# Performance work log

Measured on AMD Instinct MI355X. Metric: run time of the kernel, lower is better.

The kernel has to match this reference:

```python
import jax, jax.numpy as jnp
import numpy as np

EPS = 1e-05
NUM_HEADS = 8
NUM_GROUPS = 32  # min(32, 512 // 4)


def setup_inputs() -> dict:
    key = jax.random.key(0)
    ks = jax.random.split(key, 5)
    B, C, T, X = 4, 512, 16, 2048
    return {
        "x": jax.random.normal(ks[0], (B, C, T, X), dtype=jnp.float32),
        "gn_w": jnp.ones((C,), dtype=jnp.float32),
        "gn_b": jnp.zeros((C,), dtype=jnp.float32),
        "qkv_w": jax.random.normal(ks[1], (3 * C, C), dtype=jnp.float32) * 0.02,
        "qkv_b": jax.random.normal(ks[2], (3 * C,), dtype=jnp.float32) * 0.02,
        "proj_w": jax.random.normal(ks[3], (C, C), dtype=jnp.float32) * 1e-5,
        "proj_b": jnp.zeros((C,), dtype=jnp.float32),
        "pos_emb": jax.random.normal(ks[4], (NUM_HEADS, 2 * T), dtype=jnp.float32) * 1e-5,
    }


def _group_norm(x, w, b):
    B, C, T, X = x.shape
    g = NUM_GROUPS
    xg = x.reshape(B, g, C // g, T, X)
    mu = xg.mean(axis=(2, 3, 4), keepdims=True)
    var = ((xg - mu) ** 2).mean(axis=(2, 3, 4), keepdims=True)
    xn = ((xg - mu) * jax.lax.rsqrt(var + EPS)).reshape(B, C, T, X)
    return xn * w[None, :, None, None] + b[None, :, None, None]


def reference(x, gn_w, gn_b, qkv_w, qkv_b, proj_w, proj_b, pos_emb):
    dtype = x.dtype
    x = x.astype(jnp.float32)
    B, C, T, X = x.shape
    H = NUM_HEADS
    hc = C // H

    xn = _group_norm(x, gn_w, gn_b)
    # 1x1 conv == channel matmul: [B, 3C, T, X]
    qkv = jnp.einsum('oc,bctx->botx', qkv_w, xn) + qkv_b[None, :, None, None]
    # 'b (n heads c) t x -> n (b x) heads t c'
    qkv = qkv.reshape(B, 3, H, hc, T, X)
    qkv = qkv.transpose(1, 0, 5, 2, 4, 3).reshape(3, B * X, H, T, hc)
    q, k, v = qkv[0], qkv[1], qkv[2]

    scale = 1.0 / np.sqrt(hc)
    attn = jnp.einsum('bhqc,bhkc->bhqk', q, k * scale)  # [(B X), H, T, T]

    i = jnp.arange(T)
    pairwise = i[:, None] - i[None, :] + T - 1        # [T, T] in [0, 2T-2]
    rel = pos_emb[:, pairwise]                         # [H, T, T]

    w = jax.nn.softmax(attn + rel[None], axis=-1)
    out = jnp.einsum('bhqk,bhkc->bhcq', w, v)          # [(B X), H, hc, T]
    # '(b x) h c t -> b (h c) t x'
    out = out.reshape(B, X, H, hc, T).transpose(0, 2, 3, 4, 1).reshape(B, C, T, X)

    y = jnp.einsum('oc,bctx->botx', proj_w, out) + proj_b[None, :, None, None]
    return y.astype(dtype)
```

## Files before the change

### kernel.cpp

```cpp
#include <hip/hip_runtime.h>
#include <math.h>

#define EPSV 1e-5f

typedef _Float16 f16;
typedef _Float16 f16x8 __attribute__((ext_vector_type(8)));
typedef _Float16 f16x4 __attribute__((ext_vector_type(4)));
typedef float f32x4 __attribute__((ext_vector_type(4)));

typedef const __attribute__((address_space(1))) void* as1_cvp;
typedef __attribute__((address_space(3))) void* as3_vp;
__device__ __forceinline__ void load_lds16(const void* g, void* l) {
    __builtin_amdgcn_global_load_lds((as1_cvp)g, (as3_vp)l, 16, 0, 0);
}

static constexpr int GROUP_N = 16 * 16 * 2048;

__global__ __launch_bounds__(256) void k_xtstat(const float* __restrict__ x,
                                                f16* __restrict__ xT,
                                                float* __restrict__ psum2,
                                                float* __restrict__ psq2) {
    const int x0 = blockIdx.x * 64;
    const int c0 = blockIdx.y * 64;
    const int b  = blockIdx.z >> 4, t = blockIdx.z & 15;
    const int tid = threadIdx.x;
    __shared__ float tile[64][68];
#pragma unroll
    for (int it = 0; it < 4; ++it) {
        int idx = it * 256 + tid;
        int c = idx >> 4, xq = idx & 15;
        float4 v = *(const float4*)(x + (((size_t)(b * 512 + c0 + c) * 16 + t) * 2048) + x0 + xq * 4);
        tile[c][xq * 4 + 0] = v.x;
        tile[c][xq * 4 + 1] = v.y;
        tile[c][xq * 4 + 2] = v.z;
        tile[c][xq * 4 + 3] = v.w;
    }
    __syncthreads();
#pragma unroll
    for (int it = 0; it < 2; ++it) {
        int idx = it * 256 + tid;
        int xr = idx >> 3, ch = idx & 7;
        f16x8 h;
#pragma unroll
        for (int e = 0; e < 8; ++e) h[e] = (f16)tile[ch * 8 + e][xr];
        *(f16x8*)(xT + (((size_t)(b * 2048 + x0 + xr) * 16 + t) * 512) + c0 + ch * 8) = h;
    }
    {
        const int gg = tid >> 6, lane = tid & 63;
        float s = 0.f, q = 0.f;
#pragma unroll
        for (int i = 0; i < 16; ++i) {
            float v = tile[gg * 16 + i][lane];
            s += v; q += v * v;
        }
#pragma unroll
        for (int off = 32; off > 0; off >>= 1) {
            s += __shfl_down(s, off);
            q += __shfl_down(q, off);
        }
        if (lane == 0) {
            int grp = b * 32 + blockIdx.y * 4 + gg;
            int col = blockIdx.x * 16 + t;
            psum2[grp * 512 + col] = s;
            psq2[grp * 512 + col] = q;
        }
    }
}

__global__ void k_gn_final2(const float* __restrict__ psum2, const float* __restrict__ psq2,
                            float* __restrict__ mu, float* __restrict__ rs) {
    const int t = threadIdx.x;
    float s = 0.f, q = 0.f;
    const float* ps = psum2 + t * 512;
    const float* pq = psq2 + t * 512;
#pragma unroll 4
    for (int i = 0; i < 512; i += 4) {
        float4 a = *(const float4*)(ps + i);
        float4 c = *(const float4*)(pq + i);
        s += a.x + a.y + a.z + a.w;
        q += c.x + c.y + c.z + c.w;
    }
    const float m = s / (float)GROUP_N;
    float v = q / (float)GROUP_N - m * m;
    mu[t] = m;
    rs[t] = 1.0f / sqrtf(v + EPSV);
}

__global__ __launch_bounds__(256) void k_gn_part(const float* __restrict__ x,
                                                 float* __restrict__ psum,
                                                 float* __restrict__ psq) {
    const int blk = blockIdx.x;
    const int tid = threadIdx.x;
    const float* p = x + (size_t)blk * 32768;
    float s = 0.f, q = 0.f;
#pragma unroll
    for (int i = 0; i < 32; ++i) {
        float4 v = *(const float4*)(p + (size_t)(i * 256 + tid) * 4);
        s += v.x + v.y + v.z + v.w;
        q += v.x * v.x + v.y * v.y + v.z * v.z + v.w * v.w;
    }
#pragma unroll
    for (int off = 32; off > 0; off >>= 1) {
        s += __shfl_down(s, off);
        q += __shfl_down(q, off);
    }
    __shared__ float ls[4], lq[4];
    const int wave = tid >> 6, lane = tid & 63;
    if (lane == 0) { ls[wave] = s; lq[wave] = q; }
    __syncthreads();
    if (tid == 0) {
        psum[blk] = ls[0] + ls[1] + ls[2] + ls[3];
        psq[blk]  = lq[0] + lq[1] + lq[2] + lq[3];
    }
}

__global__ void k_gn_final(const float* __restrict__ psum, const float* __restrict__ psq,
                           float* __restrict__ mu, float* __restrict__ rs) {
    const int t = threadIdx.x;
    float s = 0.f, q = 0.f;
#pragma unroll
    for (int i = 0; i < 16; ++i) { s += psum[t * 16 + i]; q += psq[t * 16 + i]; }
    const float m = s / (float)GROUP_N;
    float v = q / (float)GROUP_N - m * m;
    mu[t] = m;
    rs[t] = 1.0f / sqrtf(v + EPSV);
}

__global__ __launch_bounds__(256) void k_fold_sc(const float* __restrict__ gn_w,
                                                 const float* __restrict__ gn_b,
                                                 const float* __restrict__ mu,
                                                 const float* __restrict__ rs,
                                                 float* __restrict__ sc,
                                                 float* __restrict__ beta) {
    const int u = blockIdx.x * 256 + threadIdx.x;
    const int b = u >> 9, c = u & 511;
    const int g = c >> 4;
    const float r = rs[b * 32 + g], m = mu[b * 32 + g];
    const float s = r * gn_w[c];
    sc[u]   = s;
    beta[u] = gn_b[c] - m * s;
}

__global__ __launch_bounds__(256) void k_fold_bias(const float* __restrict__ qkv_w,
                                                   const float* __restrict__ qkv_b,
                                                   const float* __restrict__ beta,
                                                   float* __restrict__ qbias) {
    const int u = blockIdx.x * 256 + threadIdx.x;
    const int b = u / 1536, o = u % 1536;
    float acc = qkv_b[o];
    const float* wr = qkv_w + (size_t)o * 512;
    const float* be = beta + b * 512;
#pragma unroll 4
    for (int c = 0; c < 512; c += 4) {
        float4 w4 = *(const float4*)(wr + c);
        float4 b4 = *(const float4*)(be + c);
        acc += w4.x * b4.x + w4.y * b4.y + w4.z * b4.z + w4.w * b4.w;
    }
    if (o >= 512 && o < 1024) acc *= 0.125f;
    qbias[u] = acc;
}

__global__ __launch_bounds__(256) void k_prep_wb(const float* __restrict__ qkv_w,
                                                 const float* __restrict__ sc,
                                                 f16* __restrict__ w16b) {
    const int id = blockIdx.x * 256 + threadIdx.x;
    const int b  = blockIdx.y;
    const int e0 = id * 4;
    const int o  = e0 >> 9;
    const float ksc = (o >= 512 && o < 1024) ? 0.125f : 1.0f;
    float4 wv = *(const float4*)(qkv_w + e0);
    float4 s4 = *(const float4*)(sc + b * 512 + (e0 & 511));
    f16x4 h = { (f16)(wv.x * s4.x * ksc), (f16)(wv.y * s4.y * ksc),
                (f16)(wv.z * s4.z * ksc), (f16)(wv.w * s4.w * ksc) };
    *(f16x4*)(w16b + (size_t)b * 786432 + e0) = h;
}

__global__ __launch_bounds__(256) void k_prep_p(const float* __restrict__ proj_w,
                                                f16* __restrict__ p16) {
    const int id = blockIdx.x * 256 + threadIdx.x;
    const int e0 = id * 4;
    float4 v = *(const float4*)(proj_w + e0);
    f16x4 h = { (f16)v.x, (f16)v.y, (f16)v.z, (f16)v.w };
    *(f16x4*)(p16 + e0) = h;
}

__global__ __launch_bounds__(256) void k_prep_w(const float* __restrict__ qkv_w,
                                                const float* __restrict__ proj_w,
                                                f16* __restrict__ w16,
                                                f16* __restrict__ p16) {
    const int id = blockIdx.x * 256 + threadIdx.x;
    if (id < 196608) {
        const int e0 = id * 4;
        const int o  = e0 >> 9;
        const float ksc = (o >= 512 && o < 1024) ? 0.125f : 1.0f;
        float4 v = *(const float4*)(qkv_w + e0);
        f16x4 h = { (f16)(v.x * ksc), (f16)(v.y * ksc), (f16)(v.z * ksc), (f16)(v.w * ksc) };
        *(f16x4*)(w16 + e0) = h;
    } else {
        const int e0 = (id - 196608) * 4;
        float4 v = *(const float4*)(proj_w + e0);
        f16x4 h = { (f16)v.x, (f16)v.y, (f16)v.z, (f16)v.w };
        *(f16x4*)(p16 + e0) = h;
    }
}

__global__ __launch_bounds__(256) void k_xt(const float* __restrict__ x,
                                            const float* __restrict__ sc,
                                            const float* __restrict__ beta,
                                            f16* __restrict__ xT) {
    const int x0 = blockIdx.x * 64;
    const int c0 = blockIdx.y * 64;
    const int b  = blockIdx.z >> 4, t = blockIdx.z & 15;
    const int tid = threadIdx.x;
    __shared__ float tile[64][68];
#pragma unroll
    for (int it = 0; it < 4; ++it) {
        int idx = it * 256 + tid;
        int c = idx >> 4, xq = idx & 15;
        int cg = c0 + c;
        float s = sc[b * 512 + cg], be = beta[b * 512 + cg];
        float4 v = *(const float4*)(x + (((size_t)(b * 512 + cg) * 16 + t) * 2048) + x0 + xq * 4);
        tile[c][xq * 4 + 0] = v.x * s + be;
        tile[c][xq * 4 + 1] = v.y * s + be;
        tile[c][xq * 4 + 2] = v.z * s + be;
        tile[c][xq * 4 + 3] = v.w * s + be;
    }
    __syncthreads();
#pragma unroll
    for (int it = 0; it < 2; ++it) {
        int idx = it * 256 + tid;
        int xr = idx >> 3, ch = idx & 7;
        f16x8 h;
#pragma unroll
        for (int e = 0; e < 8; ++e) h[e] = (f16)tile[ch * 8 + e][xr];
        *(f16x8*)(xT + (((size_t)(b * 2048 + x0 + xr) * 16 + t) * 512) + c0 + ch * 8) = h;
    }
}

__global__ __launch_bounds__(256) void k3_mfma(const f16* __restrict__ xT,
                                               const f16* __restrict__ wsrc,
                                               size_t w_bstride,
                                               const float* __restrict__ qkv_b,
                                               const float* __restrict__ qb_full,
                                               const float* __restrict__ pos_emb,
                                               float* __restrict__ out,
                                               f16* __restrict__ aT) {
    extern __shared__ __attribute__((aligned(16))) char smem[];
    const int h  = blockIdx.x;
    const int x0 = blockIdx.y * 8;
    const int b  = blockIdx.z;
    const int tid = threadIdx.x;
    const int lane = tid & 63, w = tid >> 6;
    const int wm = w >> 1, wn = w & 1;
    const int t_l = lane & 15, g = lane >> 4;

    const f16* xTb = xT + ((size_t)b * 2048 + x0) * 16 * 512;
    const f16* Wb  = wsrc + (size_t)b * w_bstride;

    const int l8 = lane >> 3;
    const int gc = (lane & 7) ^ l8;

    f32x4 acc[6][4];
#pragma unroll
    for (int mi = 0; mi < 6; ++mi)
#pragma unroll
        for (int ni = 0; ni < 4; ++ni) acc[mi][ni] = (f32x4){0.f, 0.f, 0.f, 0.f};

    {
#pragma unroll
        for (int i = 0; i < 6; ++i) {
            int m0 = (w * 6 + i) * 8;
            int m = m0 + l8;
            int o = (m >> 6) * 512 + h * 64 + (m & 63);
            load_lds16(Wb + (size_t)o * 512 + gc * 8, smem + m0 * 128);
        }
#pragma unroll
        for (int i = 0; i < 4; ++i) {
            int n0 = (w * 4 + i) * 8;
            int n = n0 + l8;
            load_lds16(xTb + (size_t)n * 512 + gc * 8, smem + 24576 + n0 * 128);
        }
    }
    __syncthreads();

    int cur = 0;
    for (int ks = 0; ks < 8; ++ks) {
        if (ks < 7) {
            char* bufn = smem + (cur ^ 1) * 40960;
            const int kon = (ks + 1) * 64;
#pragma unroll
            for (int i = 0; i < 6; ++i) {
                int m0 = (w * 6 + i) * 8;
                int m = m0 + l8;
                int o = (m >> 6) * 512 + h * 64 + (m & 63);
                load_lds16(Wb + (size_t)o * 512 + kon + gc * 8, bufn + m0 * 128);
            }
#pragma unroll
            for (int i = 0; i < 4; ++i) {
                int n0 = (w * 4 + i) * 8;
                int n = n0 + l8;
                load_lds16(xTb + (size_t)n * 512 + kon + gc * 8, bufn + 24576 + n0 * 128);
            }
        }
        const char* bufc = smem + cur * 40960;
        const f16* a_s = (const f16*)bufc;
        const f16* b_s = (const f16*)(bufc + 24576);
#pragma unroll
        for (int kk = 0; kk < 2; ++kk) {
            const int kb = kk * 4 + g;
            f16x8 af[6], bf[4];
#pragma unroll
            for (int mi = 0; mi < 6; ++mi) {
                int m = wm * 96 + mi * 16 + t_l;
                af[mi] = *(const f16x8*)(a_s + m * 64 + ((kb ^ (m & 7)) * 8));
            }
#pragma unroll
            for (int ni = 0; ni < 4; ++ni) {
                int n = wn * 64 + ni * 16 + t_l;
                bf[ni] = *(const f16x8*)(b_s + n * 64 + ((kb ^ (n & 7)) * 8));
            }
#pragma unroll
            for (int mi = 0; mi < 6; ++mi)
#pragma unroll
                for (int ni = 0; ni < 4; ++ni)
                    acc[mi][ni] = __builtin_amdgcn_mfma_f32_16x16x32_f16(af[mi], bf[ni], acc[mi][ni], 0, 0, 0);
        }
        __syncthreads();
        cur ^= 1;
    }

    if (qb_full) {
        const float* qb = qb_full + b * 1536;
#pragma unroll
        for (int mi = 0; mi < 6; ++mi)
#pragma unroll
            for (int ni = 0; ni < 4; ++ni) {
                int n  = wn * 64 + ni * 16 + t_l;
                int mb = wm * 96 + mi * 16 + g * 4;
                int byte_off = n * 512 + (((mb >> 6) * 8 + (((mb >> 3) & 7) ^ (n & 7))) * 16) + (mb & 7) * 2;
                f16x4 hv;
#pragma unroll
                for (int r2 = 0; r2 < 4; ++r2) {
                    int row = mb + r2;
                    hv[r2] = (f16)(acc[mi][ni][r2] + qb[(row >> 6) * 512 + h * 64 + (row & 63)]);
                }
                *(f16x4*)(smem + byte_off) = hv;
            }
    } else {
#pragma unroll
        for (int mi = 0; mi < 6; ++mi)
#pragma unroll
            for (int ni = 0; ni < 4; ++ni) {
                int n  = wn * 64 + ni * 16 + t_l;
                int mb = wm * 96 + mi * 16 + g * 4;
                int byte_off = n * 512 + (((mb >> 6) * 8 + (((mb >> 3) & 7) ^ (n & 7))) * 16) + (mb & 7) * 2;
                f16x4 hv;
#pragma unroll
                for (int r2 = 0; r2 < 4; ++r2) {
                    int row = mb + r2;
                    int reg = row >> 6;
                    float qb = qkv_b[reg * 512 + h * 64 + (row & 63)];
                    if (reg == 1) qb *= 0.125f;
                    hv[r2] = (f16)(acc[mi][ni][r2] + qb);
                }
                *(f16x4*)(smem + byte_off) = hv;
            }
    }
    __syncthreads();

#pragma unroll
    for (int xc = 0; xc < 2; ++xc) {
        const int xx = w * 2 + xc;
        const int nb = xx * 16;
        const int nrow = nb + t_l;
        const int rbase = nrow * 512;
        const int sw = nrow & 7;

        f32x4 s_acc = {0.f, 0.f, 0.f, 0.f};
#pragma unroll
        for (int half = 0; half < 2; ++half) {
            int qiA = (g + 4 * half) & 7;
            f16x8 afr = *(const f16x8*)(smem + rbase + ((8 + (qiA ^ sw)) * 16));
            f16x8 bfr = *(const f16x8*)(smem + rbase + ((qiA ^ sw) * 16));
            s_acc = __builtin_amdgcn_mfma_f32_16x16x32_f16(afr, bfr, s_acc, 0, 0, 0);
        }
        float sv[4];
#pragma unroll
        for (int r2 = 0; r2 < 4; ++r2)
            sv[r2] = s_acc[r2] + pos_emb[h * 32 + t_l - (g * 4 + r2) + 15];
        float mx = fmaxf(fmaxf(sv[0], sv[1]), fmaxf(sv[2], sv[3]));
        mx = fmaxf(mx, __shfl_xor(mx, 16));
        mx = fmaxf(mx, __shfl_xor(mx, 32));
        float es[4], ssum = 0.f;
#pragma unroll
        for (int r2 = 0; r2 < 4; ++r2) { es[r2] = __expf(sv[r2] - mx); ssum += es[r2]; }
        ssum += __shfl_xor(ssum, 16);
        ssum += __shfl_xor(ssum, 32);
        const float inv = 1.0f / ssum;
        f16x4 pfrag;
#pragma unroll
        for (int r2 = 0; r2 < 4; ++r2) pfrag[r2] = (f16)(es[r2] * inv);

        f32x4 o_acc[4];
#pragma unroll
        for (int cb = 0; cb < 4; ++cb) {
            int mV = 128 + cb * 16 + t_l;
            int qiV = (mV >> 3) & 7;
            f16x4 vfrag;
#pragma unroll
            for (int jj2 = 0; jj2 < 4; ++jj2) {
                int nV = nb + g * 4 + jj2;
                vfrag[jj2] = *(const f16*)(smem + nV * 512 + ((16 + (qiV ^ (nV & 7))) * 16) + (mV & 7) * 2);
            }
            f32x4 z = {0.f, 0.f, 0.f, 0.f};
            o_acc[cb] = __builtin_amdgcn_mfma_f32_16x16x16f16(vfrag, pfrag, z, 0, 0, 0);
        }
        if (aT) {
            f16* dst = aT + (((size_t)(b * 2048 + x0 + xx) * 16) + t_l) * 512 + h * 64;
#pragma unroll
            for (int cb = 0; cb < 4; ++cb) {
                f16x4 hv;
#pragma unroll
                for (int r2 = 0; r2 < 4; ++r2) hv[r2] = (f16)o_acc[cb][r2];
                *(f16x4*)(dst + cb * 16 + g * 4) = hv;
            }
        } else {
#pragma unroll
            for (int cb = 0; cb < 4; ++cb) {
                int qd = cb * 4 + g;
                int byte_off = rbase + (((qd >> 3) * 8 + ((qd & 7) ^ sw)) * 16);
                *(f32x4*)(smem + byte_off) = o_acc[cb];
            }
        }
    }
    if (!aT) {
        __syncthreads();
        const int c = tid & 63, tq = tid >> 6;
        const int qc = c >> 2;
#pragma unroll
        for (int ti = 0; ti < 4; ++ti) {
            int t = tq * 4 + ti;
            float vals[8];
#pragma unroll
            for (int xx = 0; xx < 8; ++xx) {
                int n2 = xx * 16 + t;
                vals[xx] = *(const float*)(smem + n2 * 512 + (((qc >> 3) * 8 + ((qc & 7) ^ (n2 & 7))) * 16) + (c & 3) * 4);
            }
            float4 lo = {vals[0], vals[1], vals[2], vals[3]};
            float4 hi = {vals[4], vals[5], vals[6], vals[7]};
            size_t oaddr = (((size_t)b * 512 + h * 64 + c) * 16 + t) * 2048 + x0;
            *(float4*)(out + oaddr) = lo;
            *(float4*)(out + oaddr + 4) = hi;
        }
    }
}

__global__ __launch_bounds__(256) void k4x(const f16* __restrict__ attnT,
                                           const f16* __restrict__ p16,
                                           const float* __restrict__ pb,
                                           float* __restrict__ out) {
    extern __shared__ __attribute__((aligned(16))) char smem[];
    const int oc  = blockIdx.x;
    const int win = blockIdx.y;
    const int b   = blockIdx.z;
    const int tid = threadIdx.x;
    const int lane = tid & 63, w = tid >> 6;
    const int t_l = lane & 15, g = lane >> 4;
    const int l8 = lane >> 3;
    const int gc = (lane & 7) ^ l8;

    const f16* Bb = attnT + ((size_t)b * 2048 + win * 16) * 16 * 512;
    const f16* Ab = p16 + (size_t)oc * 64 * 512;

    f32x4 acc[4][4];
#pragma unroll
    for (int mi = 0; mi < 4; ++mi)
#pragma unroll
        for (int ni = 0; ni < 4; ++ni) acc[mi][ni] = (f32x4){0.f, 0.f, 0.f, 0.f};

    {
#pragma unroll
        for (int i = 0; i < 2; ++i) {
            int m0 = w * 16 + i * 8;
            load_lds16(Ab + (size_t)(m0 + l8) * 512 + gc * 8, smem + m0 * 128);
        }
#pragma unroll
        for (int i = 0; i < 8; ++i) {
            int n0 = w * 64 + i * 8;
            load_lds16(Bb + (size_t)(n0 + l8) * 512 + gc * 8, smem + 8192 + n0 * 128);
        }
    }
    __syncthreads();

    int cur = 0;
    for (int ks = 0; ks < 8; ++ks) {
        if (ks < 7) {
            char* bufn = smem + (cur ^ 1) * 40960;
            const int kon = (ks + 1) * 64;
#pragma unroll
            for (int i = 0; i < 2; ++i) {
                int m0 = w * 16 + i * 8;
                load_lds16(Ab + (size_t)(m0 + l8) * 512 + kon + gc * 8, bufn + m0 * 128);
            }
#pragma unroll
            for (int i = 0; i < 8; ++i) {
                int n0 = w * 64 + i * 8;
                load_lds16(Bb + (size_t)(n0 + l8) * 512 + kon + gc * 8, bufn + 8192 + n0 * 128);
            }
        }
        const char* bufc = smem + cur * 40960;
        const f16* a_s = (const f16*)bufc;
        const f16* b_s = (const f16*)(bufc + 8192);
#pragma unroll
        for (int kk = 0; kk < 2; ++kk) {
            const int kb = kk * 4 + g;
            f16x8 af[4], bf[4];
#pragma unroll
            for (int mi = 0; mi < 4; ++mi) {
                int m = mi * 16 + t_l;
                af[mi] = *(const f16x8*)(a_s + m * 64 + ((kb ^ (m & 7)) * 8));
            }
#pragma unroll
            for (int ni = 0; ni < 4; ++ni) {
                int n = w * 64 + ni * 16 + t_l;
                bf[ni] = *(const f16x8*)(b_s + n * 64 + ((kb ^ (n & 7)) * 8));
            }
#pragma unroll
            for (int mi = 0; mi < 4; ++mi)
#pragma unroll
                for (int ni = 0; ni < 4; ++ni)
                    acc[mi][ni] = __builtin_amdgcn_mfma_f32_16x16x32_f16(af[mi], bf[ni], acc[mi][ni], 0, 0, 0);
        }
        __syncthreads();
        cur ^= 1;
    }

    float* y_s = (float*)smem;
#pragma unroll
    for (int mi = 0; mi < 4; ++mi)
#pragma unroll
        for (int ni = 0; ni < 4; ++ni) {
            int nn = w * 64 + ni * 16 + t_l;
            int xx = nn >> 4, tt = nn & 15;
            int ob = mi * 16 + g * 4;
#pragma unroll
            for (int r2 = 0; r2 < 4; ++r2)
                y_s[(ob + r2) * 273 + xx * 17 + tt] = acc[mi][ni][r2];
        }
    __syncthreads();
#pragma unroll
    for (int k = 0; k < 4; ++k) {
        int pair = k * 256 + tid;
        int o = pair >> 4, t = pair & 15;
        float bias = pb[oc * 64 + o];
        float v[16];
#pragma unroll
        for (int xx = 0; xx < 16; ++xx) v[xx] = y_s[o * 273 + xx * 17 + t] + bias;
        size_t addr = (((size_t)b * 512 + oc * 64 + o) * 16 + t) * 2048 + win * 16;
#pragma unroll
        for (int v4 = 0; v4 < 4; ++v4) {
            float4 ov = {v[v4 * 4 + 0], v[v4 * 4 + 1], v[v4 * 4 + 2], v[v4 * 4 + 3]};
            *(float4*)(out + addr + v4 * 4) = ov;
        }
    }
}


__global__ __launch_bounds__(256) void k_qkv_attn(const float* __restrict__ x,
                                                  const float* __restrict__ qkv_w,
                                                  const float* __restrict__ sc,
                                                  const float* __restrict__ qbias,
                                                  const float* __restrict__ pos_emb,
                                                  float* __restrict__ out) {
    const int h  = blockIdx.x;
    const int x0 = blockIdx.y * 4;
    const int b  = blockIdx.z;
    const int tid = threadIdx.x;

    __shared__ float a_s[192][68];
    __shared__ float b_s[64][68];
    __shared__ float w_s[4][16][17];

    const int ty = tid >> 3;
    const int tx = tid & 7;

    float acc[6][8];
#pragma unroll
    for (int j = 0; j < 6; ++j)
#pragma unroll
        for (int k = 0; k < 8; ++k) acc[j][k] = 0.f;

    for (int ko = 0; ko < 512; ko += 64) {
        __syncthreads();
#pragma unroll
        for (int it = 0; it < 12; ++it) {
            int idx = it * 256 + tid;
            int m = idx >> 4;
            int c4 = (idx & 15) * 4;
            int g = m >> 6, i = m & 63;
            int o = g * 512 + h * 64 + i;
            float4 w4 = *(const float4*)(qkv_w + (size_t)o * 512 + ko + c4);
            float4 s4 = *(const float4*)(sc + b * 512 + ko + c4);
            float ksc = (g == 1) ? 0.125f : 1.0f;
            float4 v;
            v.x = w4.x * s4.x * ksc; v.y = w4.y * s4.y * ksc;
            v.z = w4.z * s4.z * ksc; v.w = w4.w * s4.w * ksc;
            *(float4*)&a_s[m][c4] = v;
        }
#pragma unroll
        for (int it = 0; it < 4; ++it) {
            int idx = it * 256 + tid;
            int cc = idx >> 4, t = idx & 15;
            float4 v = *(const float4*)(x + ((size_t)((b * 512 + ko + cc) * 16 + t)) * 2048 + x0);
            *(float4*)&b_s[cc][t * 4] = v;
        }
        __syncthreads();
#pragma unroll 4
        for (int cc = 0; cc < 64; ++cc) {
            float av[6];
#pragma unroll
            for (int j = 0; j < 6; ++j) av[j] = a_s[ty * 6 + j][cc];
            float4 b0 = *(const float4*)&b_s[cc][tx * 8];
            float4 b1 = *(const float4*)&b_s[cc][tx * 8 + 4];
            float bv[8] = {b0.x, b0.y, b0.z, b0.w, b1.x, b1.y, b1.z, b1.w};
#pragma unroll
            for (int j = 0; j < 6; ++j)
#pragma unroll
                for (int k = 0; k < 8; ++k)
                    acc[j][k] = fmaf(av[j], bv[k], acc[j][k]);
        }
    }
#pragma unroll
    for (int j = 0; j < 6; ++j) {
        int m = ty * 6 + j;
        int o = (m >> 6) * 512 + h * 64 + (m & 63);
        float qb = qbias[b * 1536 + o];
#pragma unroll
        for (int k = 0; k < 8; ++k) acc[j][k] += qb;
    }
    __syncthreads();
#pragma unroll
    for (int j = 0; j < 6; ++j)
#pragma unroll
        for (int k = 0; k < 8; ++k)
            a_s[ty * 6 + j][tx * 8 + k] = acc[j][k];
    __syncthreads();

    {
        const int xx = tid >> 6;
        const int t  = (tid >> 2) & 15;
        const int uq = tid & 3;
        float l[4] = {0.f, 0.f, 0.f, 0.f};
        for (int i = 0; i < 64; ++i) {
            float qv = a_s[i][t * 4 + xx];
#pragma unroll
            for (int uu = 0; uu < 4; ++uu)
                l[uu] = fmaf(qv, a_s[64 + i][(uq * 4 + uu) * 4 + xx], l[uu]);
        }
#pragma unroll
        for (int uu = 0; uu < 4; ++uu) {
            int u = uq * 4 + uu;
            w_s[xx][t][u] = l[uu] + pos_emb[h * 32 + t - u + 15];
        }
    }
    __syncthreads();
    if (tid < 64) {
        const int xx = tid >> 4, t = tid & 15;
        float mx = -3.4e38f;
#pragma unroll
        for (int u = 0; u < 16; ++u) mx = fmaxf(mx, w_s[xx][t][u]);
        float ssum = 0.f;
#pragma unroll
        for (int u = 0; u < 16; ++u) {
            float e = __expf(w_s[xx][t][u] - mx);
            w_s[xx][t][u] = e;
            ssum += e;
        }
        float inv = 1.0f / ssum;
#pragma unroll
        for (int u = 0; u < 16; ++u) w_s[xx][t][u] *= inv;
    }
    __syncthreads();
    {
        const int i  = tid & 63;
        const int t4 = tid >> 6;
        float4 varr[16];
#pragma unroll
        for (int u = 0; u < 16; ++u) varr[u] = *(const float4*)&a_s[128 + i][u * 4];
#pragma unroll
        for (int tt = 0; tt < 4; ++tt) {
            int t = t4 * 4 + tt;
            float4 o4 = {0.f, 0.f, 0.f, 0.f};
#pragma unroll
            for (int u = 0; u < 16; ++u) {
                o4.x = fmaf(w_s[0][t][u], varr[u].x, o4.x);
                o4.y = fmaf(w_s[1][t][u], varr[u].y, o4.y);
                o4.z = fmaf(w_s[2][t][u], varr[u].z, o4.z);
                o4.w = fmaf(w_s[3][t][u], varr[u].w, o4.w);
            }
            *(float4*)(out + ((size_t)((b * 512 + h * 64 + i) * 16 + t)) * 2048 + x0) = o4;
        }
    }
}

__global__ __launch_bounds__(256) void k_proj(const float* __restrict__ pw,
                                              const float* __restrict__ pb,
                                              float* __restrict__ io) {
    const int n0 = blockIdx.x * 32;
    const int b  = blockIdx.y;
    const int tid = threadIdx.x;
    __shared__ float in_s[512][36];
    __shared__ float w_s[128][65];

    {
        const float* src = io + (size_t)b * 512 * 32768 + n0;
#pragma unroll
        for (int it = 0; it < 64; ++it) {
            int idx = it * 256 + tid;
            int r = idx >> 5, j = idx & 31;
            in_s[r][j] = src[(size_t)r * 32768 + j];
        }
    }
    __syncthreads();

    const int ty = tid >> 3;
    const int tx = tid & 7;

    for (int mo = 0; mo < 512; mo += 128) {
        float acc[4][4];
#pragma unroll
        for (int j = 0; j < 4; ++j)
#pragma unroll
            for (int k = 0; k < 4; ++k) acc[j][k] = 0.f;

        for (int ko = 0; ko < 512; ko += 64) {
#pragma unroll
            for (int it = 0; it < 32; ++it) {
                int idx = it * 256 + tid;
                int m = idx >> 6, cc = idx & 63;
                w_s[m][cc] = pw[(size_t)(mo + m) * 512 + ko + cc];
            }
            __syncthreads();
#pragma unroll 4
            for (int cc = 0; cc < 64; ++cc) {
                float4 bv = *(const float4*)&in_s[ko + cc][tx * 4];
                float a0 = w_s[ty * 4 + 0][cc];
                float a1 = w_s[ty * 4 + 1][cc];
                float a2 = w_s[ty * 4 + 2][cc];
                float a3 = w_s[ty * 4 + 3][cc];
                acc[0][0] = fmaf(a0, bv.x, acc[0][0]); acc[0][1] = fmaf(a0, bv.y, acc[0][1]);
                acc[0][2] = fmaf(a0, bv.z, acc[0][2]); acc[0][3] = fmaf(a0, bv.w, acc[0][3]);
                acc[1][0] = fmaf(a1, bv.x, acc[1][0]); acc[1][1] = fmaf(a1, bv.y, acc[1][1]);
                acc[1][2] = fmaf(a1, bv.z, acc[1][2]); acc[1][3] = fmaf(a1, bv.w, acc[1][3]);
                acc[2][0] = fmaf(a2, bv.x, acc[2][0]); acc[2][1] = fmaf(a2, bv.y, acc[2][1]);
                acc[2][2] = fmaf(a2, bv.z, acc[2][2]); acc[2][3] = fmaf(a2, bv.w, acc[2][3]);
                acc[3][0] = fmaf(a3, bv.x, acc[3][0]); acc[3][1] = fmaf(a3, bv.y, acc[3][1]);
                acc[3][2] = fmaf(a3, bv.z, acc[3][2]); acc[3][3] = fmaf(a3, bv.w, acc[3][3]);
            }
            __syncthreads();
        }
#pragma unroll
        for (int j = 0; j < 4; ++j) {
            int m = mo + ty * 4 + j;
            float bias = pb[m];
            float4 o4 = {acc[j][0] + bias, acc[j][1] + bias, acc[j][2] + bias, acc[j][3] + bias};
            *(float4*)(io + (size_t)(b * 512 + m) * 32768 + n0 + tx * 4) = o4;
        }
    }
}

extern "C" void kernel_launch(void* const* d_in, const int* in_sizes, int n_in,
                              void* d_out, int out_size, void* d_ws, size_t ws_size,
                              hipStream_t stream) {
    (void)in_sizes; (void)n_in; (void)out_size;
    const float* x       = (const float*)d_in[0];
    const float* gn_w    = (const float*)d_in[1];
    const float* gn_b    = (const float*)d_in[2];
    const float* qkv_w   = (const float*)d_in[3];
    const float* qkv_b   = (const float*)d_in[4];
    const float* proj_w  = (const float*)d_in[5];
    const float* proj_b  = (const float*)d_in[6];
    const float* pos_emb = (const float*)d_in[7];
    float* out = (float*)d_out;

    float* ws    = (float*)d_ws;
    float* psum  = ws;
    float* psq   = ws + 2048;
    float* mu    = ws + 4096;
    float* rs    = ws + 4224;
    float* sc    = ws + 4352;
    float* beta  = ws + 6400;
    float* qbias = ws + 8448;

    const size_t XT_BYTES = (size_t)4 * 2048 * 16 * 512 * 2;

    const size_t W16B_OFF = 65536;
    const size_t P16B_OFF = W16B_OFF + (size_t)4 * 1536 * 512 * 2;
    const size_t XT1_OFF  = P16B_OFF + (size_t)512 * 512 * 2;
    const size_t AT1_OFF  = XT1_OFF + XT_BYTES;
    const size_t NEED_T1  = AT1_OFF + XT_BYTES;

    const size_t W16_OFF = 65536;
    const size_t P16_OFF = W16_OFF + (size_t)1536 * 512 * 2;
    const size_t XT2_OFF = P16_OFF + (size_t)512 * 512 * 2;
    const size_t AT2_OFF = XT2_OFF + XT_BYTES;
    const size_t NEED_T2 = AT2_OFF + XT_BYTES;

    const int K_LDS = 81920;
    hipError_t a1 = hipFuncSetAttribute((const void*)k3_mfma,
                                        hipFuncAttributeMaxDynamicSharedMemorySize, K_LDS);
    hipError_t a2 = hipFuncSetAttribute((const void*)k4x,
                                        hipFuncAttributeMaxDynamicSharedMemorySize, K_LDS);

    if (ws_size >= NEED_T1 && a1 == hipSuccess && a2 == hipSuccess) {
        f16* w16b  = (f16*)((char*)d_ws + W16B_OFF);
        f16* p16   = (f16*)((char*)d_ws + P16B_OFF);
        f16* xT    = (f16*)((char*)d_ws + XT1_OFF);
        f16* attnT = (f16*)((char*)d_ws + AT1_OFF);
        float* psum2 = (float*)((char*)d_ws + AT1_OFF);
        float* psq2  = (float*)((char*)d_ws + AT1_OFF + 262144);
        k_xtstat<<<dim3(32, 8, 64), dim3(256), 0, stream>>>(x, xT, psum2, psq2);
        k_gn_final2<<<dim3(1), dim3(128), 0, stream>>>(psum2, psq2, mu, rs);
        k_fold_sc<<<dim3(8), dim3(256), 0, stream>>>(gn_w, gn_b, mu, rs, sc, beta);
        k_fold_bias<<<dim3(24), dim3(256), 0, stream>>>(qkv_w, qkv_b, beta, qbias);
        k_prep_wb<<<dim3(768, 4), dim3(256), 0, stream>>>(qkv_w, sc, w16b);
        k_prep_p<<<dim3(256), dim3(256), 0, stream>>>(proj_w, p16);
        k3_mfma<<<dim3(8, 256, 4), dim3(256), K_LDS, stream>>>(xT, w16b, (size_t)786432,
                                                               qkv_b, qbias, pos_emb, out, attnT);
        k4x<<<dim3(8, 128, 4), dim3(256), K_LDS, stream>>>(attnT, p16, proj_b, out);
    } else if (ws_size >= NEED_T2 && a1 == hipSuccess && a2 == hipSuccess) {
        f16* w16   = (f16*)((char*)d_ws + W16_OFF);
        f16* p16   = (f16*)((char*)d_ws + P16_OFF);
        f16* xT    = (f16*)((char*)d_ws + XT2_OFF);
        f16* attnT = (f16*)((char*)d_ws + AT2_OFF);
        k_gn_part<<<dim3(2048), dim3(256), 0, stream>>>(x, psum, psq);
        k_gn_final<<<dim3(1), dim3(128), 0, stream>>>(psum, psq, mu, rs);
        k_fold_sc<<<dim3(8), dim3(256), 0, stream>>>(gn_w, gn_b, mu, rs, sc, beta);
        k_prep_w<<<dim3(1024), dim3(256), 0, stream>>>(qkv_w, proj_w, w16, p16);
        k_xt<<<dim3(32, 8, 64), dim3(256), 0, stream>>>(x, sc, beta, xT);
        k3_mfma<<<dim3(8, 256, 4), dim3(256), K_LDS, stream>>>(xT, w16, (size_t)0,
                                                               qkv_b, nullptr, pos_emb, out, attnT);
        k4x<<<dim3(8, 128, 4), dim3(256), K_LDS, stream>>>(attnT, p16, proj_b, out);
    } else {
        k_gn_part<<<dim3(2048), dim3(256), 0, stream>>>(x, psum, psq);
        k_gn_final<<<dim3(1), dim3(128), 0, stream>>>(psum, psq, mu, rs);
        k_fold_sc<<<dim3(8), dim3(256), 0, stream>>>(gn_w, gn_b, mu, rs, sc, beta);
        k_fold_bias<<<dim3(24), dim3(256), 0, stream>>>(qkv_w, qkv_b, beta, qbias);
        k_qkv_attn<<<dim3(8, 512, 4), dim3(256), 0, stream>>>(x, qkv_w, sc, qbias, pos_emb, out);
        k_proj<<<dim3(1024, 4), dim3(256), 0, stream>>>(proj_w, proj_b, out);
    }
}
```

Measured before the change: 609.5 us.

## Double k3_mfma tile to 16 x-positions with 512-thread blocks

The fused QKV+attention kernel now processes 16 x positions per block with 8 waves instead of 8 positions with 4 waves. Each loaded weight slice is therefore reused across twice as many tokens, which halves the W reloads from global memory. LDS per block grows to 128 KB and launch bounds force one block per CU, which may reduce latency hiding. The unused direct-output path through out is removed and the kernel always writes attnT.

```diff
diff --git a/kernel.cpp b/kernel.cpp
--- a/kernel.cpp
+++ b/kernel.cpp
@@ -237,28 +237,27 @@
     }
 }
 
-__global__ __launch_bounds__(256) void k3_mfma(const f16* __restrict__ xT,
-                                               const f16* __restrict__ wsrc,
-                                               size_t w_bstride,
-                                               const float* __restrict__ qkv_b,
-                                               const float* __restrict__ qb_full,
-                                               const float* __restrict__ pos_emb,
-                                               float* __restrict__ out,
-                                               f16* __restrict__ aT) {
+__global__ __launch_bounds__(512, 1) void k3_mfma(const f16* __restrict__ xT,
+                                                  const f16* __restrict__ wsrc,
+                                                  size_t w_bstride,
+                                                  const float* __restrict__ qkv_b,
+                                                  const float* __restrict__ qb_full,
+                                                  const float* __restrict__ pos_emb,
+                                                  f16* __restrict__ aT) {
     extern __shared__ __attribute__((aligned(16))) char smem[];
     const int h  = blockIdx.x;
-    const int x0 = blockIdx.y * 8;
+    const int x0 = blockIdx.y * 16;
     const int b  = blockIdx.z;
     const int tid = threadIdx.x;
     const int lane = tid & 63, w = tid >> 6;
-    const int wm = w >> 1, wn = w & 1;
+    const int wm = w >> 2, wn = w & 3;
     const int t_l = lane & 15, g = lane >> 4;
 
     const f16* xTb = xT + ((size_t)b * 2048 + x0) * 16 * 512;
     const f16* Wb  = wsrc + (size_t)b * w_bstride;
 
-    const int l8 = lane >> 3;
-    const int gc = (lane & 7) ^ l8;
+    const int l8 = (tid >> 3) & 7;
+    const int gc = (tid & 7) ^ l8;
 
     f32x4 acc[6][4];
 #pragma unroll
@@ -268,17 +267,17 @@
 
     {
 #pragma unroll
-        for (int i = 0; i < 6; ++i) {
-            int m0 = (w * 6 + i) * 8;
-            int m = m0 + l8;
+        for (int it = 0; it < 3; ++it) {
+            int s = it * 512 + tid;
+            int m = s >> 3;
             int o = (m >> 6) * 512 + h * 64 + (m & 63);
-            load_lds16(Wb + (size_t)o * 512 + gc * 8, smem + m0 * 128);
-        }
-#pragma unroll
-        for (int i = 0; i < 4; ++i) {
-            int n0 = (w * 4 + i) * 8;
-            int n = n0 + l8;
-            load_lds16(xTb + (size_t)n * 512 + gc * 8, smem + 24576 + n0 * 128);
+            load_lds16(Wb + (size_t)o * 512 + gc * 8, smem + s * 16);
+        }
+#pragma unroll
+        for (int it = 0; it < 4; ++it) {
+            int s = it * 512 + tid;
+            int n = s >> 3;
+            load_lds16(xTb + (size_t)n * 512 + gc * 8, smem + 24576 + s * 16);
         }
     }
     __syncthreads();
@@ -286,23 +285,23 @@
     int cur = 0;
     for (int ks = 0; ks < 8; ++ks) {
         if (ks < 7) {
-            char* bufn = smem + (cur ^ 1) * 40960;
+            char* bufn = smem + (cur ^ 1) * 57344;
             const int kon = (ks + 1) * 64;
 #pragma unroll
-            for (int i = 0; i < 6; ++i) {
-                int m0 = (w * 6 + i) * 8;
-                int m = m0 + l8;
+            for (int it = 0; it < 3; ++it) {
+                int s = it * 512 + tid;
+                int m = s >> 3;
                 int o = (m >> 6) * 512 + h * 64 + (m & 63);
-                load_lds16(Wb + (size_t)o * 512 + kon + gc * 8, bufn + m0 * 128);
-            }
-#pragma unroll
-            for (int i = 0; i < 4; ++i) {
-                int n0 = (w * 4 + i) * 8;
-                int n = n0 + l8;
-                load_lds16(xTb + (size_t)n * 512 + kon + gc * 8, bufn + 24576 + n0 * 128);
-            }
-        }
-        const char* bufc = smem + cur * 40960;
+                load_lds16(Wb + (size_t)o * 512 + kon + gc * 8, bufn + s * 16);
+            }
+#pragma unroll
+            for (int it = 0; it < 4; ++it) {
+                int s = it * 512 + tid;
+                int n = s >> 3;
+                load_lds16(xTb + (size_t)n * 512 + kon + gc * 8, bufn + 24576 + s * 16);
+            }
+        }
+        const char* bufc = smem + cur * 57344;
         const f16* a_s = (const f16*)bufc;
         const f16* b_s = (const f16*)(bufc + 24576);
 #pragma unroll
@@ -415,42 +414,13 @@
             f32x4 z = {0.f, 0.f, 0.f, 0.f};
             o_acc[cb] = __builtin_amdgcn_mfma_f32_16x16x16f16(vfrag, pfrag, z, 0, 0, 0);
         }
-        if (aT) {
-            f16* dst = aT + (((size_t)(b * 2048 + x0 + xx) * 16) + t_l) * 512 + h * 64;
-#pragma unroll
-            for (int cb = 0; cb < 4; ++cb) {
-                f16x4 hv;
-#pragma unroll
-                for (int r2 = 0; r2 < 4; ++r2) hv[r2] = (f16)o_acc[cb][r2];
-                *(f16x4*)(dst + cb * 16 + g * 4) = hv;
-            }
-        } else {
-#pragma unroll
-            for (int cb = 0; cb < 4; ++cb) {
-                int qd = cb * 4 + g;
-                int byte_off = rbase + (((qd >> 3) * 8 + ((qd & 7) ^ sw)) * 16);
-                *(f32x4*)(smem + byte_off) = o_acc[cb];
-            }
-        }
-    }
-    if (!aT) {
-        __syncthreads();
-        const int c = tid & 63, tq = tid >> 6;
-        const int qc = c >> 2;
-#pragma unroll
-        for (int ti = 0; ti < 4; ++ti) {
-            int t = tq * 4 + ti;
-            float vals[8];
-#pragma unroll
-            for (int xx = 0; xx < 8; ++xx) {
-                int n2 = xx * 16 + t;
-                vals[xx] = *(const float*)(smem + n2 * 512 + (((qc >> 3) * 8 + ((qc & 7) ^ (n2 & 7))) * 16) + (c & 3) * 4);
-            }
-            float4 lo = {vals[0], vals[1], vals[2], vals[3]};
-            float4 hi = {vals[4], vals[5], vals[6], vals[7]};
-            size_t oaddr = (((size_t)b * 512 + h * 64 + c) * 16 + t) * 2048 + x0;
-            *(float4*)(out + oaddr) = lo;
-            *(float4*)(out + oaddr + 4) = hi;
+        f16* dst = aT + (((size_t)(b * 2048 + x0 + xx) * 16) + t_l) * 512 + h * 64;
+#pragma unroll
+        for (int cb = 0; cb < 4; ++cb) {
+            f16x4 hv;
+#pragma unroll
+            for (int r2 = 0; r2 < 4; ++r2) hv[r2] = (f16)o_acc[cb][r2];
+            *(f16x4*)(dst + cb * 16 + g * 4) = hv;
         }
     }
 }
@@ -806,11 +776,12 @@
     const size_t AT2_OFF = XT2_OFF + XT_BYTES;
     const size_t NEED_T2 = AT2_OFF + XT_BYTES;
 
-    const int K_LDS = 81920;
+    const int K3_LDS = 131072;
+    const int K4_LDS = 81920;
     hipError_t a1 = hipFuncSetAttribute((const void*)k3_mfma,
-                                        hipFuncAttributeMaxDynamicSharedMemorySize, K_LDS);
+                                        hipFuncAttributeMaxDynamicSharedMemorySize, K3_LDS);
     hipError_t a2 = hipFuncSetAttribute((const void*)k4x,
-                                        hipFuncAttributeMaxDynamicSharedMemorySize, K_LDS);
+                                        hipFuncAttributeMaxDynamicSharedMemorySize, K4_LDS);
 
     if (ws_size >= NEED_T1 && a1 == hipSuccess && a2 == hipSuccess) {
         f16* w16b  = (f16*)((char*)d_ws + W16B_OFF);
@@ -825,9 +796,9 @@
         k_fold_bias<<<dim3(24), dim3(256), 0, stream>>>(qkv_w, qkv_b, beta, qbias);
         k_prep_wb<<<dim3(768, 4), dim3(256), 0, stream>>>(qkv_w, sc, w16b);
         k_prep_p<<<dim3(256), dim3(256), 0, stream>>>(proj_w, p16);
-        k3_mfma<<<dim3(8, 256, 4), dim3(256), K_LDS, stream>>>(xT, w16b, (size_t)786432,
-                                                               qkv_b, qbias, pos_emb, out, attnT);
-        k4x<<<dim3(8, 128, 4), dim3(256), K_LDS, stream>>>(attnT, p16, proj_b, out);
+        k3_mfma<<<dim3(8, 128, 4), dim3(512), K3_LDS, stream>>>(xT, w16b, (size_t)786432,
+                                                                qkv_b, qbias, pos_emb, attnT);
+        k4x<<<dim3(8, 128, 4), dim3(256), K4_LDS, stream>>>(attnT, p16, proj_b, out);
     } else if (ws_size >= NEED_T2 && a1 == hipSuccess && a2 == hipSuccess) {
         f16* w16   = (f16*)((char*)d_ws + W16_OFF);
         f16* p16   = (f16*)((char*)d_ws + P16_OFF);
@@ -838,9 +809,9 @@
         k_fold_sc<<<dim3(8), dim3(256), 0, stream>>>(gn_w, gn_b, mu, rs, sc, beta);
         k_prep_w<<<dim3(1024), dim3(256), 0, stream>>>(qkv_w, proj_w, w16, p16);
         k_xt<<<dim3(32, 8, 64), dim3(256), 0, stream>>>(x, sc, beta, xT);
-        k3_mfma<<<dim3(8, 256, 4), dim3(256), K_LDS, stream>>>(xT, w16, (size_t)0,
-                                                               qkv_b, nullptr, pos_emb, out, attnT);
-        k4x<<<dim3(8, 128, 4), dim3(256), K_LDS, stream>>>(attnT, p16, proj_b, out);
+        k3_mfma<<<dim3(8, 128, 4), dim3(512), K3_LDS, stream>>>(xT, w16, (size_t)0,
+                                                                qkv_b, nullptr, pos_emb, attnT);
+        k4x<<<dim3(8, 128, 4), dim3(256), K4_LDS, stream>>>(attnT, p16, proj_b, out);
     } else {
         k_gn_part<<<dim3(2048), dim3(256), 0, stream>>>(x, psum, psq);
         k_gn_final<<<dim3(1), dim3(128), 0, stream>>>(psum, psq, mu, rs);
```

Result: slower. 627.6 us (+3.0%).
